# Kernel optimization log

Hardware: AMD Instinct MI355X
Metric: run time of the kernel (lower is better)

## Reference

```python
import jax, jax.numpy as jnp
import numpy as np

_DN = ('NCHW', 'OIHW', 'NCHW')

def _conv(x, w, stride=1, pad=1, dil=1, groups=1):
    return jax.lax.conv_general_dilated(
        x, w, window_strides=(stride, stride),
        padding=[(pad, pad), (pad, pad)],
        rhs_dilation=(dil, dil),
        feature_group_count=groups,
        dimension_numbers=_DN)


def setup_inputs() -> dict:
    key = jax.random.key(0)
    k1, k2, k3 = jax.random.split(key, 3)
    B, T, C_in, H, W = 4, 16, 32, 64, 64
    hidden = 64
    x = jax.random.normal(k1, (B, T, C_in, H, W), dtype=jnp.float32)
    # input-to-hidden conv weight: 3 gates stacked along out channels
    fan_i = C_in * 3 * 3
    W_i = jax.random.normal(k2, (3 * hidden, C_in, 3, 3), dtype=jnp.float32) / np.sqrt(fan_i)
    fan_h = hidden * 3 * 3
    W_h = jax.random.normal(k3, (3 * hidden, hidden, 3, 3), dtype=jnp.float32) / np.sqrt(fan_h)
    return {"x": x, "W_i": W_i, "W_h": W_h}


def reference(x, W_i, W_h):
    # x: [B, T, C_in, H, W] (batch_first). Single-layer unidirectional ConvGRU.
    B, T, C_in, H, Wd = x.shape
    hidden = W_h.shape[1]

    def cell(h, x_t):
        gi = _conv(x_t, W_i)          # [B, 3*hidden, H, W]
        gh = _conv(h, W_h)            # [B, 3*hidden, H, W]
        i_r, i_z, i_n = jnp.split(gi, 3, axis=1)
        h_r, h_z, h_n = jnp.split(gh, 3, axis=1)
        r = jax.nn.sigmoid(i_r + h_r)
        z = jax.nn.sigmoid(i_z + h_z)
        n = jnp.tanh(i_n + r * h_n)
        h_new = (1.0 - z) * n + z * h
        return h_new, h_new

    h0 = jnp.zeros((B, hidden, H, Wd), dtype=x.dtype)
    xs = jnp.moveaxis(x, 1, 0)        # [T, B, C_in, H, W]
    _, hs = jax.lax.scan(cell, h0, xs)
    return jnp.moveaxis(hs, 0, 1)     # [B, T, hidden, H, W]
```

## Files before the change

kernel.cpp:

```cpp
#include <hip/hip_runtime.h>
#include <math.h>

constexpr int B_  = 4;
constexpr int T_  = 16;
constexpr int CIN = 32;
constexpr int HID = 64;
constexpr int HH  = 64;
constexpr int WW  = 64;
constexpr int HW  = HH * WW;

constexpr int TR = 8,  TC = 16;
constexpr int PR = TR + 2, PC = TC + 2;
constexpr int CSL = 40;
constexpr int KCH = 32;
constexpr int ASLAB_HW  = 3 * 36 * 16 * 8;
constexpr int ATOTAL    = 12 * ASLAB_HW;
constexpr int TIN_HW    = PR * PC * CSL;
constexpr int TIN_GRAN  = TIN_HW / 8;
constexpr int ROW_HW    = 66 * CSL;
constexpr int PIMG_HW   = 66 * ROW_HW;

constexpr size_t A2_HW    = (size_t)ATOTAL;
constexpr size_t XT_OFF   = A2_HW;
constexpr size_t XT_HW    = (size_t)64 * PIMG_HW;
constexpr size_t HT_OFF   = XT_OFF + XT_HW;
constexpr size_t HTBUF_HW = (size_t)8 * PIMG_HW;
constexpr size_t WS_NEED_BYTES = (A2_HW + XT_HW + 2 * HTBUF_HW) * 2;

constexpr int PB_XFILL = 66 * 64;
constexpr int PB_WCONV = (ATOTAL + 255) / 256;
constexpr int HZ_GRAN  = (int)(2 * HTBUF_HW / 8);
constexpr int PB_HZERO = (HZ_GRAN + 255) / 256;
constexpr int PB_TOTAL = PB_XFILL + PB_WCONV + PB_HZERO;

typedef __attribute__((ext_vector_type(8))) short bf16x8;
typedef __attribute__((ext_vector_type(4))) float f32x4;

#define GLOAD_LDS16(gsrc, ldst) \
  __builtin_amdgcn_global_load_lds((const __attribute__((address_space(1))) void*)(gsrc), \
                                   (__attribute__((address_space(3))) void*)(ldst), 16, 0, 0)

__device__ inline unsigned short f2bf(float f) {
    union { float f; unsigned u; } v; v.f = f;
    return (unsigned short)((v.u + 0x7FFFu + ((v.u >> 16) & 1u)) >> 16);
}
__device__ inline float bf2f(unsigned short h) {
    union { unsigned u; float f; } v; v.u = (unsigned)h << 16; return v.f;
}

__global__ void prep(const float* __restrict__ x,
                     const float* __restrict__ Wi, const float* __restrict__ Wh,
                     unsigned short* __restrict__ A2,
                     unsigned short* __restrict__ xT,
                     unsigned short* __restrict__ hT) {
    __shared__ float lds[64 * 41];
    const int bid = blockIdx.x;

    if (bid < PB_XFILL) {
        const int riT = bid % 66;
        const int bt  = bid / 66;
        unsigned short* dst = xT + (size_t)bt * PIMG_HW + (size_t)riT * ROW_HW;
        const bool interior = (riT >= 1 && riT <= 64);
        if (interior) {
            const float* src = x + (size_t)bt * 32 * HW + (riT - 1) * WW;
            const int p = threadIdx.x & 63;
            #pragma unroll
            for (int j = 0; j < 8; ++j) {
                int c = j * 4 + (threadIdx.x >> 6);
                lds[p * 41 + c] = src[c * HW + p];
            }
        }
        __syncthreads();
        for (int g = threadIdx.x; g < ROW_HW / 8; g += 256) {
            bf16x8 vv;
            #pragma unroll
            for (int k = 0; k < 8; ++k) {
                int off = g * 8 + k;
                int px = off / CSL, slot = off - px * CSL;
                float v = 0.f;
                if (interior && slot < 32 && px >= 1 && px <= 64)
                    v = lds[(px - 1) * 41 + slot];
                vv[k] = (short)f2bf(v);
            }
            *(bf16x8*)(dst + g * 8) = vv;
        }
    } else if (bid < PB_XFILL + PB_WCONV) {
        int idx = (bid - PB_XFILL) * 256 + threadIdx.x;
        if (idx >= ATOTAL) return;
        int ic  = idx & 31;
        int r1  = idx >> 5;
        int tap = r1 % 9;
        int r2  = r1 / 9;
        int m   = r2 & 15;
        int r3  = r2 >> 4;
        int gt  = r3 % 3;
        int r4  = r3 / 3;
        int hg  = r4 & 3;
        int ch  = r4 >> 2;
        int o   = gt * 64 + hg * 16 + m;
        float w = (ch == 0) ? Wi[(o * CIN + ic) * 9 + tap]
                            : Wh[(o * HID + (ch - 1) * 32 + ic) * 9 + tap];
        size_t dst = (size_t)(ch * 4 + hg) * ASLAB_HW
                   + ((size_t)(gt * 36 + tap * 4 + (ic >> 3)) * 16 + m) * 8 + (ic & 7);
        A2[dst] = f2bf(w);
    } else {
        int i = (bid - PB_XFILL - PB_WCONV) * 256 + threadIdx.x;
        if (i < HZ_GRAN) ((f32x4*)hT)[i] = f32x4{0.f, 0.f, 0.f, 0.f};
    }
}

__global__ __launch_bounds__(256, 2) void convgru_mfma(
    const unsigned short* __restrict__ xT,
    const unsigned short* __restrict__ A2,
    const unsigned short* __restrict__ hTrd,
    unsigned short* __restrict__ hTwr,
    float* __restrict__ out, int t)
{
    __shared__ __align__(16) unsigned short t0s[TIN_HW];
    __shared__ __align__(16) unsigned short t1s[TIN_HW];
    __shared__ __align__(16) unsigned short t2s[TIN_HW];

    const int tid  = threadIdx.x;
    const int lane = tid & 63, wave = tid >> 6;
    const int px   = lane & 15, kl = lane >> 4;
    const int ty = blockIdx.x >> 2, tx = blockIdx.x & 3;
    const int hg = blockIdx.y, b = blockIdx.z;
    const int gy0 = ty * TR, gx0 = tx * TC;

    const unsigned short* xs = xT + (size_t)(b * T_ + t) * PIMG_HW;
    const int rowbase = gy0 * 66 + gx0;

    f32x4 accR[2] = {}, accZ[2] = {}, accNX[2] = {}, accNH[2] = {};
    bf16x8 a[27];

    auto stage_tin = [&](const unsigned short* src, unsigned short* dst) {
        #pragma unroll
        for (int j = 0; j < 4; ++j) {
            int G = tid + j * 256;
            if (G < TIN_GRAN) {
                int r = G / 90, w = G - 90 * r;
                GLOAD_LDS16(src + (size_t)(rowbase + r * 66) * CSL + w * 8, dst + G * 8);
            }
        }
    };
    auto regA = [&](int ch) {
        const unsigned short* s = A2 + (size_t)(ch * 4 + hg) * ASLAB_HW + lane * 8;
        #pragma unroll
        for (int i = 0; i < 27; ++i)
            a[i] = *(const bf16x8*)(s + (size_t)((i / 9) * 36 + (i % 9) * 4) * 128);
    };

    const int rb = (wave * 2 * PC + px) * CSL + kl * 8;

    auto compute = [&](const unsigned short* tb, bool isX, const unsigned short* nextA) {
        bf16x8 P[4][3];
        #pragma unroll
        for (int r = 0; r < 4; ++r)
            #pragma unroll
            for (int s = 0; s < 3; ++s)
                P[r][s] = *(const bf16x8*)(tb + rb + (r * PC + s) * CSL);
        #pragma unroll
        for (int dy = 0; dy < 3; ++dy) {
            #pragma unroll
            for (int dx = 0; dx < 3; ++dx) {
                const int tap = dy * 3 + dx;
                bf16x8 b0 = P[dy][dx], b1 = P[dy + 1][dx];
                bf16x8 ar = a[tap], az = a[9 + tap], an = a[18 + tap];
                if (nextA) {
                    a[tap]      = *(const bf16x8*)(nextA + (size_t)(0 * 36 + tap * 4) * 128);
                    a[9 + tap]  = *(const bf16x8*)(nextA + (size_t)(1 * 36 + tap * 4) * 128);
                    a[18 + tap] = *(const bf16x8*)(nextA + (size_t)(2 * 36 + tap * 4) * 128);
                }
                accR[0] = __builtin_amdgcn_mfma_f32_16x16x32_bf16(ar, b0, accR[0], 0, 0, 0);
                accR[1] = __builtin_amdgcn_mfma_f32_16x16x32_bf16(ar, b1, accR[1], 0, 0, 0);
                accZ[0] = __builtin_amdgcn_mfma_f32_16x16x32_bf16(az, b0, accZ[0], 0, 0, 0);
                accZ[1] = __builtin_amdgcn_mfma_f32_16x16x32_bf16(az, b1, accZ[1], 0, 0, 0);
                if (isX) {
                    accNX[0] = __builtin_amdgcn_mfma_f32_16x16x32_bf16(an, b0, accNX[0], 0, 0, 0);
                    accNX[1] = __builtin_amdgcn_mfma_f32_16x16x32_bf16(an, b1, accNX[1], 0, 0, 0);
                } else {
                    accNH[0] = __builtin_amdgcn_mfma_f32_16x16x32_bf16(an, b0, accNH[0], 0, 0, 0);
                    accNH[1] = __builtin_amdgcn_mfma_f32_16x16x32_bf16(an, b1, accNH[1], 0, 0, 0);
                }
            }
        }
    };

    stage_tin(xs, t0s);
    if (t > 0) {
        stage_tin(hTrd + (size_t)(b * 2 + 0) * PIMG_HW, t1s);
        stage_tin(hTrd + (size_t)(b * 2 + 1) * PIMG_HW, t2s);
    }
    regA(0);
    __syncthreads();

    const unsigned short* A1p = (t > 0)
        ? A2 + (size_t)(1 * 4 + hg) * ASLAB_HW + lane * 8 : nullptr;
    const unsigned short* A2p = (t > 0)
        ? A2 + (size_t)(2 * 4 + hg) * ASLAB_HW + lane * 8 : nullptr;

    compute(t0s, true, A1p);
    if (t > 0) {
        compute(t1s, false, A2p);
        compute(t2s, false, nullptr);
    }

    float* outp = out + ((size_t)(b * T_ + t)) * HID * HW;
    const int c0   = hg * 16 + kl * 4;
    const int slot = c0 & 31;
    const unsigned short* hbuf = (hg < 2) ? t1s : t2s;
    #pragma unroll
    for (int g = 0; g < 2; ++g) {
        int gy = gy0 + wave * 2 + g;
        int gx = gx0 + px;
        float hvf[4] = {0.f, 0.f, 0.f, 0.f};
        if (t > 0) {
            const unsigned short* hp =
                hbuf + ((wave * 2 + g + 1) * PC + (px + 1)) * CSL + slot;
            #pragma unroll
            for (int q = 0; q < 4; ++q) hvf[q] = bf2f(hp[q]);
        }
        unsigned short hvals[4];
        #pragma unroll
        for (int q = 0; q < 4; ++q) {
            int c = c0 + q;
            float sr = __builtin_amdgcn_rcpf(1.f + __expf(-accR[g][q]));
            float sz = __builtin_amdgcn_rcpf(1.f + __expf(-accZ[g][q]));
            float ag = accNX[g][q] + sr * accNH[g][q];
            float nn = 2.f * __builtin_amdgcn_rcpf(1.f + __expf(-2.f * ag)) - 1.f;
            float hn = nn + sz * (hvf[q] - nn);
            outp[(size_t)c * HW + gy * WW + gx] = hn;
            hvals[q] = f2bf(hn);
        }
        unsigned short* hd = hTwr + (size_t)(b * 2 + (c0 >> 5)) * PIMG_HW
                           + (size_t)((gy + 1) * 66 + (gx + 1)) * CSL + slot;
        *(uint2*)hd = *(const uint2*)hvals;
    }
}

constexpr int F_AROWB = 640;
constexpr int R4_ASLAB = 48 * 9 * KCH;
constexpr int R4_AVEC  = R4_ASLAB / 8;
constexpr int R4_ATOT  = 12 * R4_ASLAB;
__global__ void wconv_r4(const float* __restrict__ Wi, const float* __restrict__ Wh,
                         unsigned short* __restrict__ A2) {
    int idx = blockIdx.x * 256 + threadIdx.x;
    if (idx >= R4_ATOT) return;
    int ic = idx & 31; int r1 = idx >> 5;
    int tap = r1 % 9; int r2 = r1 / 9;
    int m = r2 & 15; int r3 = r2 >> 4;
    int gt = r3 % 3; int r4 = r3 / 3;
    int hg = r4 & 3; int ch = r4 >> 2;
    int o = gt * 64 + hg * 16 + m;
    float w = (ch == 0) ? Wi[(o * CIN + ic) * 9 + tap]
                        : Wh[(o * HID + (ch - 1) * 32 + ic) * 9 + tap];
    A2[idx] = f2bf(w);
}
__global__ __launch_bounds__(256, 2) void convgru_r4(
    const float* __restrict__ x, const unsigned short* __restrict__ A2,
    const float* hall, float* out, int t)
{
    __shared__ __align__(16) unsigned short tin[PR * PC * 40];
    __shared__ __align__(16) unsigned short Alr[48 * (F_AROWB / 2)];
    const int tid = threadIdx.x;
    const int lane = tid & 63, wave = tid >> 6;
    const int px = lane & 15, kl = lane >> 4;
    const int ty = blockIdx.x >> 2, tx = blockIdx.x & 3;
    const int hg = blockIdx.y, b = blockIdx.z;
    const int gy0 = ty * TR, gx0 = tx * TC;
    const int nch = (t > 0) ? 3 : 1;
    const float* hb = (t > 0) ? (hall + ((size_t)(b * T_ + t - 1)) * HID * HW) : nullptr;
    const float* xb = x + ((size_t)(b * T_ + t)) * CIN * HW;
    f32x4 accR[2] = {}, accZ[2] = {}, accNX[2] = {}, accNH[2] = {};
    float ireg[23]; bf16x8 areg[7];
    auto load_in = [&](int ch) {
        const float* src = (ch == 0) ? xb : (hb + (size_t)(ch - 1) * KCH * HW);
        #pragma unroll
        for (int j = 0; j < 23; ++j) {
            int e = tid + j * 256; float v = 0.f;
            if (e < PR * PC * KCH) {
                int ic = e / (PR * PC); int rem = e - ic * (PR * PC);
                int r = rem / PC, c = rem - r * PC;
                int gy = gy0 + r - 1, gx = gx0 + c - 1;
                if ((unsigned)gy < (unsigned)HH && (unsigned)gx < (unsigned)WW)
                    v = src[ic * HW + gy * WW + gx];
            }
            ireg[j] = v;
        }
    };
    auto load_Ar = [&](int ch) {
        const unsigned short* s = A2 + (size_t)(ch * 4 + hg) * R4_ASLAB;
        #pragma unroll
        for (int j = 0; j < 7; ++j) { int v = tid + j * 256; if (v < R4_AVEC) areg[j] = *(const bf16x8*)(s + v * 8); }
    };
    auto write_in = [&]() {
        #pragma unroll
        for (int j = 0; j < 23; ++j) {
            int e = tid + j * 256;
            if (e < PR * PC * KCH) {
                int ic = e / (PR * PC); int rem = e - ic * (PR * PC);
                int r = rem / PC, c = rem - r * PC;
                tin[(r * PC + c) * 40 + ic] = f2bf(ireg[j]);
            }
        }
    };
    auto write_Ar = [&]() {
        #pragma unroll
        for (int j = 0; j < 7; ++j) {
            int v = tid + j * 256;
            if (v < R4_AVEC) {
                int row = v / 36; int kb = (v - row * 36) * 16;
                char* dst = (char*)Alr + row * F_AROWB + (kb ^ ((row & 7) << 4));
                *(bf16x8*)dst = areg[j];
            }
        }
    };
    const int rb0 = ((wave * 2 + 0) * PC + px) * 40 + kl * 8;
    const int rb1 = rb0 + PC * 40;
    const int swA = (px & 7) << 4;
    auto compute = [&](bool isX) {
        #pragma unroll
        for (int tap = 0; tap < 9; ++tap) {
            const int dy = tap / 3, dx = tap - 3 * dy;
            const int toff = (dy * PC + dx) * 40;
            bf16x8 b0 = *(const bf16x8*)(tin + rb0 + toff);
            bf16x8 b1 = *(const bf16x8*)(tin + rb1 + toff);
            const char* ab = (const char*)Alr + px * F_AROWB + ((tap * 64 + kl * 16) ^ swA);
            bf16x8 ar = *(const bf16x8*)(ab);
            bf16x8 az = *(const bf16x8*)(ab + 16 * F_AROWB);
            bf16x8 an = *(const bf16x8*)(ab + 32 * F_AROWB);
            accR[0] = __builtin_amdgcn_mfma_f32_16x16x32_bf16(ar, b0, accR[0], 0, 0, 0);
            accR[1] = __builtin_amdgcn_mfma_f32_16x16x32_bf16(ar, b1, accR[1], 0, 0, 0);
            accZ[0] = __builtin_amdgcn_mfma_f32_16x16x32_bf16(az, b0, accZ[0], 0, 0, 0);
            accZ[1] = __builtin_amdgcn_mfma_f32_16x16x32_bf16(az, b1, accZ[1], 0, 0, 0);
            if (isX) {
                accNX[0] = __builtin_amdgcn_mfma_f32_16x16x32_bf16(an, b0, accNX[0], 0, 0, 0);
                accNX[1] = __builtin_amdgcn_mfma_f32_16x16x32_bf16(an, b1, accNX[1], 0, 0, 0);
            } else {
                accNH[0] = __builtin_amdgcn_mfma_f32_16x16x32_bf16(an, b0, accNH[0], 0, 0, 0);
                accNH[1] = __builtin_amdgcn_mfma_f32_16x16x32_bf16(an, b1, accNH[1], 0, 0, 0);
            }
        }
    };
    load_in(0); load_Ar(0); write_in(); write_Ar();
    __syncthreads();
    for (int ch = 0; ch < nch; ++ch) {
        if (ch + 1 < nch) { load_in(ch + 1); load_Ar(ch + 1); }
        compute(ch == 0);
        __syncthreads();
        if (ch + 1 < nch) { write_in(); write_Ar(); __syncthreads(); }
    }
    float* outp = out + ((size_t)(b * T_ + t)) * HID * HW;
    #pragma unroll
    for (int g = 0; g < 2; ++g) {
        int gy = gy0 + wave * 2 + g; int gx = gx0 + px;
        #pragma unroll
        for (int q = 0; q < 4; ++q) {
            int c = hg * 16 + kl * 4 + q;
            float sr = 1.f / (1.f + expf(-accR[g][q]));
            float sz = 1.f / (1.f + expf(-accZ[g][q]));
            float nn = tanhf(accNX[g][q] + sr * accNH[g][q]);
            float hv = hb ? hb[(size_t)c * HW + gy * WW + gx] : 0.f;
            outp[(size_t)c * HW + gy * WW + gx] = (1.f - sz) * nn + sz * hv;
        }
    }
}

extern "C" void kernel_launch(void* const* d_in, const int* in_sizes, int n_in,
                              void* d_out, int out_size, void* d_ws, size_t ws_size,
                              hipStream_t stream) {
    const float* x  = (const float*)d_in[0];
    const float* Wi = (const float*)d_in[1];
    const float* Wh = (const float*)d_in[2];
    float* out = (float*)d_out;

    if (ws_size >= WS_NEED_BYTES) {
        unsigned short* A2  = (unsigned short*)d_ws;
        unsigned short* xT  = A2 + XT_OFF;
        unsigned short* hT0 = A2 + HT_OFF;
        unsigned short* hT1 = hT0 + HTBUF_HW;

        prep<<<PB_TOTAL, 256, 0, stream>>>(x, Wi, Wh, A2, xT, hT0);
        for (int t = 0; t < T_; ++t) {
            unsigned short* rd = (t & 1) ? hT1 : hT0;
            unsigned short* wr = (t & 1) ? hT0 : hT1;
            convgru_mfma<<<dim3(32, 4, 4), 256, 0, stream>>>(xT, A2, rd, wr, out, t);
        }
    } else {
        unsigned short* A2 = (unsigned short*)d_ws;
        wconv_r4<<<(R4_ATOT + 255) / 256, 256, 0, stream>>>(Wi, Wh, A2);
        for (int t = 0; t < T_; ++t)
            convgru_r4<<<dim3(32, 4, 4), 256, 0, stream>>>(x, A2, out, out, t);
    }
}
```

Before: 166.7 us.

## Fuse two GRU timesteps per launch using halo recompute of hidden state

```diff
diff --git a/kernel.cpp b/kernel.cpp
--- a/kernel.cpp
+++ b/kernel.cpp
@@ -1,5 +1,9 @@
 #include <hip/hip_runtime.h>
 #include <math.h>
+
+typedef unsigned short us;
+typedef __attribute__((ext_vector_type(8))) short bf16x8;
+typedef __attribute__((ext_vector_type(4))) float f32x4;
 
 constexpr int B_  = 4;
 constexpr int T_  = 16;
@@ -9,60 +13,55 @@
 constexpr int WW  = 64;
 constexpr int HW  = HH * WW;
 
-constexpr int TR = 8,  TC = 16;
-constexpr int PR = TR + 2, PC = TC + 2;
 constexpr int CSL = 40;
-constexpr int KCH = 32;
-constexpr int ASLAB_HW  = 3 * 36 * 16 * 8;
-constexpr int ATOTAL    = 12 * ASLAB_HW;
-constexpr int TIN_HW    = PR * PC * CSL;
-constexpr int TIN_GRAN  = TIN_HW / 8;
-constexpr int ROW_HW    = 66 * CSL;
-constexpr int PIMG_HW   = 66 * ROW_HW;
-
-constexpr size_t A2_HW    = (size_t)ATOTAL;
-constexpr size_t XT_OFF   = A2_HW;
+constexpr int ASLAB_HW = 3 * 36 * 16 * 8;
+constexpr int ATOTAL   = 12 * ASLAB_HW;
+constexpr int PD       = 68;
+constexpr int PROW_HW  = PD * CSL;
+constexpr int PIMG_HW  = PD * PROW_HW;
+constexpr int T20_HW = 8 * 20 * CSL;
+constexpr int T18_HW = 6 * 18 * CSL;
+constexpr int T20_GR = T20_HW / 8;
+constexpr int T18_GR = T18_HW / 8;
+
+constexpr size_t XT_OFF   = (size_t)ATOTAL;
 constexpr size_t XT_HW    = (size_t)64 * PIMG_HW;
 constexpr size_t HT_OFF   = XT_OFF + XT_HW;
 constexpr size_t HTBUF_HW = (size_t)8 * PIMG_HW;
-constexpr size_t WS_NEED_BYTES = (A2_HW + XT_HW + 2 * HTBUF_HW) * 2;
-
-constexpr int PB_XFILL = 66 * 64;
+constexpr size_t WS_NEED_BYTES = (HT_OFF + 2 * HTBUF_HW) * 2;
+
+constexpr int PB_XFILL = PD * 64;
 constexpr int PB_WCONV = (ATOTAL + 255) / 256;
 constexpr int HZ_GRAN  = (int)(2 * HTBUF_HW / 8);
 constexpr int PB_HZERO = (HZ_GRAN + 255) / 256;
 constexpr int PB_TOTAL = PB_XFILL + PB_WCONV + PB_HZERO;
 
-typedef __attribute__((ext_vector_type(8))) short bf16x8;
-typedef __attribute__((ext_vector_type(4))) float f32x4;
-
 #define GLOAD_LDS16(gsrc, ldst) \
   __builtin_amdgcn_global_load_lds((const __attribute__((address_space(1))) void*)(gsrc), \
                                    (__attribute__((address_space(3))) void*)(ldst), 16, 0, 0)
-
-__device__ inline unsigned short f2bf(float f) {
+#define MFMA_B(d, A, Bv) d = __builtin_amdgcn_mfma_f32_16x16x32_bf16(A, Bv, d, 0, 0, 0)
+
+__device__ inline us f2bf(float f) {
     union { float f; unsigned u; } v; v.f = f;
-    return (unsigned short)((v.u + 0x7FFFu + ((v.u >> 16) & 1u)) >> 16);
-}
-__device__ inline float bf2f(unsigned short h) {
+    return (us)((v.u + 0x7FFFu + ((v.u >> 16) & 1u)) >> 16);
+}
+__device__ inline float bf2f(us h) {
     union { unsigned u; float f; } v; v.u = (unsigned)h << 16; return v.f;
 }
 
 __global__ void prep(const float* __restrict__ x,
                      const float* __restrict__ Wi, const float* __restrict__ Wh,
-                     unsigned short* __restrict__ A2,
-                     unsigned short* __restrict__ xT,
-                     unsigned short* __restrict__ hT) {
+                     us* __restrict__ A2, us* __restrict__ xT, us* __restrict__ hT) {
     __shared__ float lds[64 * 41];
     const int bid = blockIdx.x;
 
     if (bid < PB_XFILL) {
-        const int riT = bid % 66;
-        const int bt  = bid / 66;
-        unsigned short* dst = xT + (size_t)bt * PIMG_HW + (size_t)riT * ROW_HW;
-        const bool interior = (riT >= 1 && riT <= 64);
+        const int riT = bid % PD;
+        const int bt  = bid / PD;
+        us* dst = xT + (size_t)bt * PIMG_HW + (size_t)riT * PROW_HW;
+        const bool interior = (riT >= 2 && riT <= 65);
         if (interior) {
-            const float* src = x + (size_t)bt * 32 * HW + (riT - 1) * WW;
+            const float* src = x + (size_t)bt * 32 * HW + (riT - 2) * WW;
             const int p = threadIdx.x & 63;
             #pragma unroll
             for (int j = 0; j < 8; ++j) {
@@ -71,15 +70,15 @@
             }
         }
         __syncthreads();
-        for (int g = threadIdx.x; g < ROW_HW / 8; g += 256) {
+        for (int g = threadIdx.x; g < PROW_HW / 8; g += 256) {
             bf16x8 vv;
             #pragma unroll
             for (int k = 0; k < 8; ++k) {
                 int off = g * 8 + k;
                 int px = off / CSL, slot = off - px * CSL;
                 float v = 0.f;
-                if (interior && slot < 32 && px >= 1 && px <= 64)
-                    v = lds[(px - 1) * 41 + slot];
+                if (interior && slot < 32 && px >= 2 && px <= 65)
+                    v = lds[(px - 2) * 41 + slot];
                 vv[k] = (short)f2bf(v);
             }
             *(bf16x8*)(dst + g * 8) = vv;
@@ -109,141 +108,225 @@
     }
 }
 
-__global__ __launch_bounds__(256, 2) void convgru_mfma(
-    const unsigned short* __restrict__ xT,
-    const unsigned short* __restrict__ A2,
-    const unsigned short* __restrict__ hTrd,
-    unsigned short* __restrict__ hTwr,
-    float* __restrict__ out, int t)
+__global__ __launch_bounds__(512, 2) void convgru_pair(
+    const us* __restrict__ xT, const us* __restrict__ A2g,
+    const us* __restrict__ hTrd, us* __restrict__ hTwr,
+    float* __restrict__ out, int t0)
 {
-    __shared__ __align__(16) unsigned short t0s[TIN_HW];
-    __shared__ __align__(16) unsigned short t1s[TIN_HW];
-    __shared__ __align__(16) unsigned short t2s[TIN_HW];
-
-    const int tid  = threadIdx.x;
-    const int lane = tid & 63, wave = tid >> 6;
-    const int px   = lane & 15, kl = lane >> 4;
-    const int ty = blockIdx.x >> 2, tx = blockIdx.x & 3;
-    const int hg = blockIdx.y, b = blockIdx.z;
-    const int gy0 = ty * TR, gx0 = tx * TC;
-
-    const unsigned short* xs = xT + (size_t)(b * T_ + t) * PIMG_HW;
-    const int rowbase = gy0 * 66 + gx0;
-
-    f32x4 accR[2] = {}, accZ[2] = {}, accNX[2] = {}, accNH[2] = {};
+    __shared__ __align__(16) us t20x[T20_HW], t20L[T20_HW], t20H[T20_HW];
+    __shared__ __align__(16) us t18x[T18_HW], t18L[T18_HW], t18H[T18_HW];
+
+    const int tid = threadIdx.x, lane = tid & 63, wave = tid >> 6;
+    const int hg = wave & 3, sg = wave >> 2;
+    const int px = lane & 15, kl = lane >> 4;
+    const int tile = blockIdx.x, ty = tile >> 2, tx = tile & 3, b = blockIdx.z;
+    const int gy0 = ty * 4, gx0 = tx * 16;
+
+    auto st20 = [&](const us* img, us* dst) {
+        #pragma unroll
+        for (int j = 0; j < 2; ++j) {
+            int G = tid + j * 512;
+            if (G < T20_GR) {
+                int r = G / 100, w = G - 100 * r;
+                GLOAD_LDS16(img + (size_t)((gy0 + r) * PD + gx0) * CSL + w * 8, dst + G * 8);
+            }
+        }
+    };
+    auto st18 = [&](const us* img, us* dst) {
+        #pragma unroll
+        for (int j = 0; j < 2; ++j) {
+            int G = tid + j * 512;
+            if (G < T18_GR) {
+                int r = G / 90, w = G - 90 * r;
+                GLOAD_LDS16(img + (size_t)((gy0 + 1 + r) * PD + gx0 + 1) * CSL + w * 8, dst + G * 8);
+            }
+        }
+    };
+
+    const us* A0p = A2g + (size_t)(0 * 4 + hg) * ASLAB_HW + lane * 8;
+    const us* A1p = A2g + (size_t)(1 * 4 + hg) * ASLAB_HW + lane * 8;
+    const us* A2p = A2g + (size_t)(2 * 4 + hg) * ASLAB_HW + lane * 8;
+
     bf16x8 a[27];
-
-    auto stage_tin = [&](const unsigned short* src, unsigned short* dst) {
-        #pragma unroll
-        for (int j = 0; j < 4; ++j) {
-            int G = tid + j * 256;
-            if (G < TIN_GRAN) {
-                int r = G / 90, w = G - 90 * r;
-                GLOAD_LDS16(src + (size_t)(rowbase + r * 66) * CSL + w * 8, dst + G * 8);
-            }
-        }
-    };
-    auto regA = [&](int ch) {
-        const unsigned short* s = A2 + (size_t)(ch * 4 + hg) * ASLAB_HW + lane * 8;
+    auto loadA = [&](const us* p) {
         #pragma unroll
         for (int i = 0; i < 27; ++i)
-            a[i] = *(const bf16x8*)(s + (size_t)((i / 9) * 36 + (i % 9) * 4) * 128);
-    };
-
-    const int rb = (wave * 2 * PC + px) * CSL + kl * 8;
-
-    auto compute = [&](const unsigned short* tb, bool isX, const unsigned short* nextA) {
-        bf16x8 P[4][3];
-        #pragma unroll
-        for (int r = 0; r < 4; ++r)
-            #pragma unroll
-            for (int s = 0; s < 3; ++s)
-                P[r][s] = *(const bf16x8*)(tb + rb + (r * PC + s) * CSL);
-        #pragma unroll
-        for (int dy = 0; dy < 3; ++dy) {
+            a[i] = *(const bf16x8*)(p + (size_t)((i / 9) * 36 + (i % 9) * 4) * 128);
+    };
+
+    const int rp_t[2][3] = {{0, 0, 1}, {1, 2, 2}};
+    const int co_t[2][3] = {{0, 2, 0}, {2, 0, 2}};
+
+    f32x4 aR[3][2], aZ[3][2], aNX[3][2], aNH[3][2];
+    auto zacc = [&]() {
+        #pragma unroll
+        for (int u = 0; u < 3; ++u)
+            #pragma unroll
+            for (int g = 0; g < 2; ++g) {
+                aR[u][g] = f32x4{0.f,0.f,0.f,0.f}; aZ[u][g] = f32x4{0.f,0.f,0.f,0.f};
+                aNX[u][g] = f32x4{0.f,0.f,0.f,0.f}; aNH[u][g] = f32x4{0.f,0.f,0.f,0.f};
+            }
+    };
+
+    auto phaseA = [&](const us* tb, bool isX, const us* nextA) {
+        #pragma unroll
+        for (int u = 0; u < 3; ++u) {
+            const int rp = rp_t[sg][u], co = co_t[sg][u];
+            const int rbu = (2 * rp * 20 + co + px) * CSL + kl * 8;
+            const bool pf = (u == 2) && (nextA != nullptr);
             #pragma unroll
             for (int dx = 0; dx < 3; ++dx) {
+                bf16x8 P[4];
+                #pragma unroll
+                for (int r = 0; r < 4; ++r)
+                    P[r] = *(const bf16x8*)(tb + rbu + (r * 20 + dx) * CSL);
+                #pragma unroll
+                for (int dy = 0; dy < 3; ++dy) {
+                    const int tap = dy * 3 + dx;
+                    bf16x8 b0 = P[dy], b1 = P[dy + 1];
+                    bf16x8 ar = a[tap], az = a[9 + tap], an = a[18 + tap];
+                    if (pf) {
+                        a[tap]      = *(const bf16x8*)(nextA + (size_t)(0 * 36 + tap * 4) * 128);
+                        a[9 + tap]  = *(const bf16x8*)(nextA + (size_t)(1 * 36 + tap * 4) * 128);
+                        a[18 + tap] = *(const bf16x8*)(nextA + (size_t)(2 * 36 + tap * 4) * 128);
+                    }
+                    MFMA_B(aR[u][0], ar, b0); MFMA_B(aR[u][1], ar, b1);
+                    MFMA_B(aZ[u][0], az, b0); MFMA_B(aZ[u][1], az, b1);
+                    if (isX) { MFMA_B(aNX[u][0], an, b0); MFMA_B(aNX[u][1], an, b1); }
+                    else     { MFMA_B(aNH[u][0], an, b0); MFMA_B(aNH[u][1], an, b1); }
+                }
+            }
+        }
+    };
+
+    auto phaseB = [&](const us* tb, bool isX, const us* nextA) {
+        const int rbu = (2 * sg * 18 + px) * CSL + kl * 8;
+        #pragma unroll
+        for (int dx = 0; dx < 3; ++dx) {
+            bf16x8 P[4];
+            #pragma unroll
+            for (int r = 0; r < 4; ++r)
+                P[r] = *(const bf16x8*)(tb + rbu + (r * 18 + dx) * CSL);
+            #pragma unroll
+            for (int dy = 0; dy < 3; ++dy) {
                 const int tap = dy * 3 + dx;
-                bf16x8 b0 = P[dy][dx], b1 = P[dy + 1][dx];
+                bf16x8 b0 = P[dy], b1 = P[dy + 1];
                 bf16x8 ar = a[tap], az = a[9 + tap], an = a[18 + tap];
                 if (nextA) {
                     a[tap]      = *(const bf16x8*)(nextA + (size_t)(0 * 36 + tap * 4) * 128);
                     a[9 + tap]  = *(const bf16x8*)(nextA + (size_t)(1 * 36 + tap * 4) * 128);
                     a[18 + tap] = *(const bf16x8*)(nextA + (size_t)(2 * 36 + tap * 4) * 128);
                 }
-                accR[0] = __builtin_amdgcn_mfma_f32_16x16x32_bf16(ar, b0, accR[0], 0, 0, 0);
-                accR[1] = __builtin_amdgcn_mfma_f32_16x16x32_bf16(ar, b1, accR[1], 0, 0, 0);
-                accZ[0] = __builtin_amdgcn_mfma_f32_16x16x32_bf16(az, b0, accZ[0], 0, 0, 0);
-                accZ[1] = __builtin_amdgcn_mfma_f32_16x16x32_bf16(az, b1, accZ[1], 0, 0, 0);
-                if (isX) {
-                    accNX[0] = __builtin_amdgcn_mfma_f32_16x16x32_bf16(an, b0, accNX[0], 0, 0, 0);
-                    accNX[1] = __builtin_amdgcn_mfma_f32_16x16x32_bf16(an, b1, accNX[1], 0, 0, 0);
-                } else {
-                    accNH[0] = __builtin_amdgcn_mfma_f32_16x16x32_bf16(an, b0, accNH[0], 0, 0, 0);
-                    accNH[1] = __builtin_amdgcn_mfma_f32_16x16x32_bf16(an, b1, accNH[1], 0, 0, 0);
+                MFMA_B(aR[0][0], ar, b0); MFMA_B(aR[0][1], ar, b1);
+                MFMA_B(aZ[0][0], az, b0); MFMA_B(aZ[0][1], az, b1);
+                if (isX) { MFMA_B(aNX[0][0], an, b0); MFMA_B(aNX[0][1], an, b1); }
+                else     { MFMA_B(aNH[0][0], an, b0); MFMA_B(aNH[0][1], an, b1); }
+            }
+        }
+    };
+
+    const int c0 = hg * 16 + kl * 4;
+    const int slot = c0 & 31;
+
+    const us* xs0 = xT + (size_t)(b * T_ + t0) * PIMG_HW;
+    const us* xs1 = xT + (size_t)(b * T_ + t0 + 1) * PIMG_HW;
+    st20(xs0, t20x);
+    st18(xs1, t18x);
+    if (t0 > 0) {
+        st20(hTrd + (size_t)(b * 2 + 0) * PIMG_HW, t20L);
+        st20(hTrd + (size_t)(b * 2 + 1) * PIMG_HW, t20H);
+    }
+    loadA(A0p);
+    __syncthreads();
+
+    zacc();
+    if (t0 > 0) {
+        phaseA(t20x, true,  A1p);
+        phaseA(t20L, false, A2p);
+        phaseA(t20H, false, A0p);
+    } else {
+        phaseA(t20x, true, nullptr);
+    }
+
+    {
+        float* outp = out + ((size_t)(b * T_ + t0)) * HID * HW;
+        us* hlds = (hg < 2) ? t18L : t18H;
+        const us* h20 = (hg < 2) ? t20L : t20H;
+        #pragma unroll
+        for (int u = 0; u < 3; ++u) {
+            const int rp = rp_t[sg][u], co = co_t[sg][u];
+            #pragma unroll
+            for (int g = 0; g < 2; ++g) {
+                int rr = 2 * rp + g;
+                int cc = co + px;
+                int gy = gy0 - 1 + rr, gx = gx0 - 1 + cc;
+                bool inimg = ((unsigned)gy < 64u) && ((unsigned)gx < 64u);
+                float hvf[4] = {0.f, 0.f, 0.f, 0.f};
+                if (t0 > 0) {
+                    const us* hp = h20 + (size_t)((rr + 1) * 20 + cc + 1) * CSL + slot;
+                    #pragma unroll
+                    for (int q = 0; q < 4; ++q) hvf[q] = bf2f(hp[q]);
                 }
-            }
-        }
-    };
-
-    stage_tin(xs, t0s);
-    if (t > 0) {
-        stage_tin(hTrd + (size_t)(b * 2 + 0) * PIMG_HW, t1s);
-        stage_tin(hTrd + (size_t)(b * 2 + 1) * PIMG_HW, t2s);
-    }
-    regA(0);
+                us hv[4];
+                bool inner = (rr >= 1 && rr <= 4 && cc >= 1 && cc <= 16);
+                #pragma unroll
+                for (int q = 0; q < 4; ++q) {
+                    float sr = __builtin_amdgcn_rcpf(1.f + __expf(-aR[u][g][q]));
+                    float sz = __builtin_amdgcn_rcpf(1.f + __expf(-aZ[u][g][q]));
+                    float ag = aNX[u][g][q] + sr * aNH[u][g][q];
+                    float nn = 2.f * __builtin_amdgcn_rcpf(1.f + __expf(-2.f * ag)) - 1.f;
+                    float hn = nn + sz * (hvf[q] - nn);
+                    hn = inimg ? hn : 0.f;
+                    hv[q] = f2bf(hn);
+                    if (inner) outp[(size_t)(c0 + q) * HW + gy * WW + gx] = hn;
+                }
+                *(uint2*)(hlds + (size_t)(rr * 18 + cc) * CSL + slot) = *(const uint2*)hv;
+            }
+        }
+    }
     __syncthreads();
 
-    const unsigned short* A1p = (t > 0)
-        ? A2 + (size_t)(1 * 4 + hg) * ASLAB_HW + lane * 8 : nullptr;
-    const unsigned short* A2p = (t > 0)
-        ? A2 + (size_t)(2 * 4 + hg) * ASLAB_HW + lane * 8 : nullptr;
-
-    compute(t0s, true, A1p);
-    if (t > 0) {
-        compute(t1s, false, A2p);
-        compute(t2s, false, nullptr);
-    }
-
-    float* outp = out + ((size_t)(b * T_ + t)) * HID * HW;
-    const int c0   = hg * 16 + kl * 4;
-    const int slot = c0 & 31;
-    const unsigned short* hbuf = (hg < 2) ? t1s : t2s;
-    #pragma unroll
-    for (int g = 0; g < 2; ++g) {
-        int gy = gy0 + wave * 2 + g;
-        int gx = gx0 + px;
-        float hvf[4] = {0.f, 0.f, 0.f, 0.f};
-        if (t > 0) {
-            const unsigned short* hp =
-                hbuf + ((wave * 2 + g + 1) * PC + (px + 1)) * CSL + slot;
+    zacc();
+    phaseB(t18x, true,  A1p);
+    phaseB(t18L, false, A2p);
+    phaseB(t18H, false, nullptr);
+
+    {
+        float* outp = out + ((size_t)(b * T_ + t0 + 1)) * HID * HW;
+        const us* hlds = (hg < 2) ? t18L : t18H;
+        #pragma unroll
+        for (int g = 0; g < 2; ++g) {
+            int orow = 2 * sg + g;
+            int gy = gy0 + orow, gx = gx0 + px;
+            float hvf[4];
+            const us* hp = hlds + (size_t)((orow + 1) * 18 + (px + 1)) * CSL + slot;
             #pragma unroll
             for (int q = 0; q < 4; ++q) hvf[q] = bf2f(hp[q]);
-        }
-        unsigned short hvals[4];
-        #pragma unroll
-        for (int q = 0; q < 4; ++q) {
-            int c = c0 + q;
-            float sr = __builtin_amdgcn_rcpf(1.f + __expf(-accR[g][q]));
-            float sz = __builtin_amdgcn_rcpf(1.f + __expf(-accZ[g][q]));
-            float ag = accNX[g][q] + sr * accNH[g][q];
-            float nn = 2.f * __builtin_amdgcn_rcpf(1.f + __expf(-2.f * ag)) - 1.f;
-            float hn = nn + sz * (hvf[q] - nn);
-            outp[(size_t)c * HW + gy * WW + gx] = hn;
-            hvals[q] = f2bf(hn);
-        }
-        unsigned short* hd = hTwr + (size_t)(b * 2 + (c0 >> 5)) * PIMG_HW
-                           + (size_t)((gy + 1) * 66 + (gx + 1)) * CSL + slot;
-        *(uint2*)hd = *(const uint2*)hvals;
+            us hv[4];
+            #pragma unroll
+            for (int q = 0; q < 4; ++q) {
+                float sr = __builtin_amdgcn_rcpf(1.f + __expf(-aR[0][g][q]));
+                float sz = __builtin_amdgcn_rcpf(1.f + __expf(-aZ[0][g][q]));
+                float ag = aNX[0][g][q] + sr * aNH[0][g][q];
+                float nn = 2.f * __builtin_amdgcn_rcpf(1.f + __expf(-2.f * ag)) - 1.f;
+                float hn = nn + sz * (hvf[q] - nn);
+                outp[(size_t)(c0 + q) * HW + gy * WW + gx] = hn;
+                hv[q] = f2bf(hn);
+            }
+            us* hd = hTwr + (size_t)(b * 2 + (c0 >> 5)) * PIMG_HW
+                   + (size_t)((gy + 2) * PD + (gx + 2)) * CSL + slot;
+            *(uint2*)hd = *(const uint2*)hv;
+        }
     }
 }
 
 constexpr int F_AROWB = 640;
-constexpr int R4_ASLAB = 48 * 9 * KCH;
+constexpr int R4_ASLAB = 48 * 9 * 32;
 constexpr int R4_AVEC  = R4_ASLAB / 8;
 constexpr int R4_ATOT  = 12 * R4_ASLAB;
+constexpr int FPR = 10, FPC = 18;
 __global__ void wconv_r4(const float* __restrict__ Wi, const float* __restrict__ Wh,
-                         unsigned short* __restrict__ A2) {
+                         us* __restrict__ A2) {
     int idx = blockIdx.x * 256 + threadIdx.x;
     if (idx >= R4_ATOT) return;
     int ic = idx & 31; int r1 = idx >> 5;
@@ -257,30 +340,30 @@
     A2[idx] = f2bf(w);
 }
 __global__ __launch_bounds__(256, 2) void convgru_r4(
-    const float* __restrict__ x, const unsigned short* __restrict__ A2,
+    const float* __restrict__ x, const us* __restrict__ A2,
     const float* hall, float* out, int t)
 {
-    __shared__ __align__(16) unsigned short tin[PR * PC * 40];
-    __shared__ __align__(16) unsigned short Alr[48 * (F_AROWB / 2)];
+    __shared__ __align__(16) us tin[FPR * FPC * 40];
+    __shared__ __align__(16) us Alr[48 * (F_AROWB / 2)];
     const int tid = threadIdx.x;
     const int lane = tid & 63, wave = tid >> 6;
     const int px = lane & 15, kl = lane >> 4;
     const int ty = blockIdx.x >> 2, tx = blockIdx.x & 3;
     const int hg = blockIdx.y, b = blockIdx.z;
-    const int gy0 = ty * TR, gx0 = tx * TC;
+    const int gy0 = ty * 8, gx0 = tx * 16;
     const int nch = (t > 0) ? 3 : 1;
     const float* hb = (t > 0) ? (hall + ((size_t)(b * T_ + t - 1)) * HID * HW) : nullptr;
     const float* xb = x + ((size_t)(b * T_ + t)) * CIN * HW;
     f32x4 accR[2] = {}, accZ[2] = {}, accNX[2] = {}, accNH[2] = {};
     float ireg[23]; bf16x8 areg[7];
     auto load_in = [&](int ch) {
-        const float* src = (ch == 0) ? xb : (hb + (size_t)(ch - 1) * KCH * HW);
+        const float* src = (ch == 0) ? xb : (hb + (size_t)(ch - 1) * 32 * HW);
         #pragma unroll
         for (int j = 0; j < 23; ++j) {
             int e = tid + j * 256; float v = 0.f;
-            if (e < PR * PC * KCH) {
-                int ic = e / (PR * PC); int rem = e - ic * (PR * PC);
-                int r = rem / PC, c = rem - r * PC;
+            if (e < FPR * FPC * 32) {
+                int ic = e / (FPR * FPC); int rem = e - ic * (FPR * FPC);
+                int r = rem / FPC, c = rem - r * FPC;
                 int gy = gy0 + r - 1, gx = gx0 + c - 1;
                 if ((unsigned)gy < (unsigned)HH && (unsigned)gx < (unsigned)WW)
                     v = src[ic * HW + gy * WW + gx];
@@ -289,7 +372,7 @@
         }
     };
     auto load_Ar = [&](int ch) {
-        const unsigned short* s = A2 + (size_t)(ch * 4 + hg) * R4_ASLAB;
+        const us* s = A2 + (size_t)(ch * 4 + hg) * R4_ASLAB;
         #pragma unroll
         for (int j = 0; j < 7; ++j) { int v = tid + j * 256; if (v < R4_AVEC) areg[j] = *(const bf16x8*)(s + v * 8); }
     };
@@ -297,10 +380,10 @@
         #pragma unroll
         for (int j = 0; j < 23; ++j) {
             int e = tid + j * 256;
-            if (e < PR * PC * KCH) {
-                int ic = e / (PR * PC); int rem = e - ic * (PR * PC);
-                int r = rem / PC, c = rem - r * PC;
-                tin[(r * PC + c) * 40 + ic] = f2bf(ireg[j]);
+            if (e < FPR * FPC * 32) {
+                int ic = e / (FPR * FPC); int rem = e - ic * (FPR * FPC);
+                int r = rem / FPC, c = rem - r * FPC;
+                tin[(r * FPC + c) * 40 + ic] = f2bf(ireg[j]);
             }
         }
     };
@@ -315,31 +398,24 @@
             }
         }
     };
-    const int rb0 = ((wave * 2 + 0) * PC + px) * 40 + kl * 8;
-    const int rb1 = rb0 + PC * 40;
+    const int rb0 = ((wave * 2 + 0) * FPC + px) * 40 + kl * 8;
+    const int rb1 = rb0 + FPC * 40;
     const int swA = (px & 7) << 4;
     auto compute = [&](bool isX) {
         #pragma unroll
         for (int tap = 0; tap < 9; ++tap) {
             const int dy = tap / 3, dx = tap - 3 * dy;
-            const int toff = (dy * PC + dx) * 40;
+            const int toff = (dy * FPC + dx) * 40;
             bf16x8 b0 = *(const bf16x8*)(tin + rb0 + toff);
             bf16x8 b1 = *(const bf16x8*)(tin + rb1 + toff);
             const char* ab = (const char*)Alr + px * F_AROWB + ((tap * 64 + kl * 16) ^ swA);
             bf16x8 ar = *(const bf16x8*)(ab);
             bf16x8 az = *(const bf16x8*)(ab + 16 * F_AROWB);
             bf16x8 an = *(const bf16x8*)(ab + 32 * F_AROWB);
-            accR[0] = __builtin_amdgcn_mfma_f32_16x16x32_bf16(ar, b0, accR[0], 0, 0, 0);
-            accR[1] = __builtin_amdgcn_mfma_f32_16x16x32_bf16(ar, b1, accR[1], 0, 0, 0);
-            accZ[0] = __builtin_amdgcn_mfma_f32_16x16x32_bf16(az, b0, accZ[0], 0, 0, 0);
-            accZ[1] = __builtin_amdgcn_mfma_f32_16x16x32_bf16(az, b1, accZ[1], 0, 0, 0);
-            if (isX) {
-                accNX[0] = __builtin_amdgcn_mfma_f32_16x16x32_bf16(an, b0, accNX[0], 0, 0, 0);
-                accNX[1] = __builtin_amdgcn_mfma_f32_16x16x32_bf16(an, b1, accNX[1], 0, 0, 0);
-            } else {
-                accNH[0] = __builtin_amdgcn_mfma_f32_16x16x32_bf16(an, b0, accNH[0], 0, 0, 0);
-                accNH[1] = __builtin_amdgcn_mfma_f32_16x16x32_bf16(an, b1, accNH[1], 0, 0, 0);
-            }
+            MFMA_B(accR[0], ar, b0); MFMA_B(accR[1], ar, b1);
+            MFMA_B(accZ[0], az, b0); MFMA_B(accZ[1], az, b1);
+            if (isX) { MFMA_B(accNX[0], an, b0); MFMA_B(accNX[1], an, b1); }
+            else     { MFMA_B(accNH[0], an, b0); MFMA_B(accNH[1], an, b1); }
         }
     };
     load_in(0); load_Ar(0); write_in(); write_Ar();
@@ -375,19 +451,19 @@
     float* out = (float*)d_out;
 
     if (ws_size >= WS_NEED_BYTES) {
-        unsigned short* A2  = (unsigned short*)d_ws;
-        unsigned short* xT  = A2 + XT_OFF;
-        unsigned short* hT0 = A2 + HT_OFF;
-        unsigned short* hT1 = hT0 + HTBUF_HW;
+        us* A2  = (us*)d_ws;
+        us* xT  = A2 + XT_OFF;
+        us* hT0 = A2 + HT_OFF;
+        us* hT1 = hT0 + HTBUF_HW;
 
         prep<<<PB_TOTAL, 256, 0, stream>>>(x, Wi, Wh, A2, xT, hT0);
-        for (int t = 0; t < T_; ++t) {
-            unsigned short* rd = (t & 1) ? hT1 : hT0;
-            unsigned short* wr = (t & 1) ? hT0 : hT1;
-            convgru_mfma<<<dim3(32, 4, 4), 256, 0, stream>>>(xT, A2, rd, wr, out, t);
+        for (int p = 0; p < T_ / 2; ++p) {
+            us* rd = (p & 1) ? hT1 : hT0;
+            us* wr = (p & 1) ? hT0 : hT1;
+            convgru_pair<<<dim3(64, 1, 4), 512, 0, stream>>>(xT, A2, rd, wr, out, 2 * p);
         }
     } else {
-        unsigned short* A2 = (unsigned short*)d_ws;
+        us* A2 = (us*)d_ws;
         wconv_r4<<<(R4_ATOT + 255) / 256, 256, 0, stream>>>(Wi, Wh, A2);
         for (int t = 0; t < T_; ++t)
             convgru_r4<<<dim3(32, 4, 4), 256, 0, stream>>>(x, A2, out, out, t);
```

Result: slower. 208.7 us (+25.2%).
